# Optimization experiments

Hardware: AMD Instinct MI355X
Metric: run time of the kernel (lower is better)

Reference implementation:

```python
import jax, jax.numpy as jnp
import numpy as np

B, N, D, H, DK, DV = 16, 512, 512, 8, 64, 64


def setup_inputs() -> dict:
    key = jax.random.key(0)
    ks = jax.random.split(key, 16)
    xav = lambda k, fi, fo: jax.random.uniform(k, (fi, fo), jnp.float32,
                                               -jnp.sqrt(6.0 / (fi + fo)), jnp.sqrt(6.0 / (fi + fo)))
    return {
        "queries": jax.random.normal(ks[0], (B, N, D), jnp.float32),
        "keys": jax.random.normal(ks[1], (B, N, D), jnp.float32),
        "values": jax.random.normal(ks[2], (B, N, D), jnp.float32),
        "box_relation_embed_matrix": jax.random.uniform(ks[3], (B, H, N, N), jnp.float32),
        "ExtrAtt": jax.random.normal(ks[4], (B, H, N, N), jnp.float32),
        "Wq": xav(ks[5], D, H * DK), "bq": jnp.zeros((H * DK,), jnp.float32),
        "Wk": xav(ks[6], D, H * DK), "bk": jnp.zeros((H * DK,), jnp.float32),
        "Wv": xav(ks[7], D, H * DV), "bv": jnp.zeros((H * DV,), jnp.float32),
        "Wo": xav(ks[8], H * DV, D), "bo": jnp.zeros((D,), jnp.float32),
    }


def reference(queries, keys, values, box_relation_embed_matrix, ExtrAtt,
              Wq, bq, Wk, bk, Wv, bv, Wo, bo):
    b_s, nq, _ = queries.shape
    nk = keys.shape[1]
    # projections -> [B, H, N, d]
    q = (queries @ Wq + bq).reshape(b_s, nq, H, DK).transpose(0, 2, 1, 3)
    k = (keys @ Wk + bk).reshape(b_s, nk, H, DK).transpose(0, 2, 1, 3)
    v = (values @ Wv + bv).reshape(b_s, nk, H, DV).transpose(0, 2, 1, 3)
    scale = 1.0 / jnp.sqrt(jnp.asarray(DK, queries.dtype))
    att = jnp.einsum('bhqd,bhkd->bhqk', q, k) * scale
    # log geometric (box) bias + content attention, first softmax
    w_mn = jnp.log(jnp.clip(box_relation_embed_matrix, 1e-6, None)) + att
    w_mn = jax.nn.softmax(w_mn, axis=-1)
    # dropout is identity in eval; add extra attention and re-normalize
    att2 = jax.nn.softmax(w_mn + ExtrAtt, axis=-1)
    out = jnp.einsum('bhqk,bhkd->bhqd', att2, v)
    out = out.transpose(0, 2, 1, 3).reshape(b_s, nq, H * DV)
    return out @ Wo + bo
```

## Files before the change

kernel.cpp:

```cpp
#include <hip/hip_runtime.h>
#include <hip/hip_bf16.h>

#define NB 16
#define NN 512
#define ND 512
#define NH 8

using short8 = __attribute__((ext_vector_type(8))) short;
using f32x4  = __attribute__((ext_vector_type(4))) float;

static __device__ __forceinline__ unsigned short f2bf(float f) {
  unsigned u = __builtin_bit_cast(unsigned, f);
  unsigned r = 0x7fffu + ((u >> 16) & 1u);
  return (unsigned short)((u + r) >> 16);
}
static __device__ __forceinline__ float bf2f(unsigned short u) {
  return __builtin_bit_cast(float, (unsigned)u << 16);
}
static __device__ __forceinline__ void ld_lds16(const float* g, float* l) {
  __builtin_amdgcn_global_load_lds((const __attribute__((address_space(1))) void*)g,
                                   (__attribute__((address_space(3))) void*)l, 16, 0, 0);
}

__global__ __launch_bounds__(256) void wprep(
    const float* __restrict__ Wq, const float* __restrict__ Wk,
    const float* __restrict__ Wv, const float* __restrict__ Wo,
    unsigned short* __restrict__ T) {
  const float* W;
  switch (blockIdx.z) {
    case 0: W = Wq; break;
    case 1: W = Wk; break;
    case 2: W = Wv; break;
    default: W = Wo; break;
  }
  unsigned short* Wt = T + (size_t)blockIdx.z * 512 * 512;
  __shared__ float tile[64][65];
  const int t = threadIdx.x;
  const int k0 = blockIdx.x * 64, n0 = blockIdx.y * 64;
#pragma unroll
  for (int it = 0; it < 4; ++it) {
    int row = it * 16 + (t >> 4);
    int c4 = (t & 15) * 4;
    float4 v = *(const float4*)&W[(size_t)(k0 + row) * 512 + n0 + c4];
    tile[row][c4] = v.x; tile[row][c4 + 1] = v.y;
    tile[row][c4 + 2] = v.z; tile[row][c4 + 3] = v.w;
  }
  __syncthreads();
#pragma unroll
  for (int it = 0; it < 4; ++it) {
    int nr = it * 16 + (t >> 4);
    int k4 = (t & 15) * 4;
    ushort4 o;
    o.x = f2bf(tile[k4 + 0][nr]); o.y = f2bf(tile[k4 + 1][nr]);
    o.z = f2bf(tile[k4 + 2][nr]); o.w = f2bf(tile[k4 + 3][nr]);
    *(ushort4*)&Wt[(size_t)(n0 + nr) * 512 + k0 + k4] = o;
  }
}

__global__ __launch_bounds__(256) void qkv_gemm(
    const float* __restrict__ Xq, const float* __restrict__ Xk,
    const float* __restrict__ Xv, const unsigned short* __restrict__ Wt,
    const float* __restrict__ bq, const float* __restrict__ bk,
    const float* __restrict__ bv, unsigned short* __restrict__ q_ws,
    unsigned short* __restrict__ k_ws, unsigned short* __restrict__ vt_ws) {
  const int zi = blockIdx.z;
  const float* X = (zi == 0) ? Xq : (zi == 1) ? Xk : Xv;
  const unsigned short* Wz = Wt + (size_t)zi * 512 * 512;
  const float* bias = (zi == 0) ? bq : (zi == 1) ? bk : bv;
  const int m0 = blockIdx.x * 128, n0 = blockIdx.y * 128;
  __shared__ unsigned short Al[2][128][40];
  __shared__ unsigned short Bl[2][128][40];
  const int t = threadIdx.x;
  const int w = t >> 6, l = t & 63;
  const int lr = l & 15, lg = l >> 4;
  const int wr = (w >> 1) * 64, wc = (w & 1) * 64;
  f32x4 acc[4][4] = {};
  for (int kk = 0; kk < 512; kk += 64) {
    __syncthreads();
    {
      const int colk = (t & 15) * 4;
      const int kc = colk >> 5, kin = colk & 31;
#pragma unroll
      for (int p = 0; p < 8; ++p) {
        int row = p * 16 + (t >> 4);
        float4 v = *(const float4*)&X[(size_t)(m0 + row) * 512 + kk + colk];
        ushort4 o;
        o.x = f2bf(v.x); o.y = f2bf(v.y); o.z = f2bf(v.z); o.w = f2bf(v.w);
        *(ushort4*)&Al[kc][row][kin] = o;
      }
      const int colk8 = (t & 7) * 8;
      const int kc2 = colk8 >> 5, kin2 = colk8 & 31;
#pragma unroll
      for (int p = 0; p < 4; ++p) {
        int row = p * 32 + (t >> 3);
        short8 v = *(const short8*)&Wz[(size_t)(n0 + row) * 512 + kk + colk8];
        *(short8*)&Bl[kc2][row][kin2] = v;
      }
    }
    __syncthreads();
#pragma unroll
    for (int kc = 0; kc < 2; ++kc) {
      short8 a[4], b[4];
      const int lk = lg * 8;
#pragma unroll
      for (int i = 0; i < 4; ++i) a[i] = *(const short8*)&Al[kc][wr + i * 16 + lr][lk];
#pragma unroll
      for (int i = 0; i < 4; ++i) b[i] = *(const short8*)&Bl[kc][wc + i * 16 + lr][lk];
#pragma unroll
      for (int i = 0; i < 4; ++i)
#pragma unroll
        for (int j = 0; j < 4; ++j)
          acc[i][j] = __builtin_amdgcn_mfma_f32_16x16x32_bf16(a[i], b[j], acc[i][j], 0, 0, 0);
    }
  }
#pragma unroll
  for (int j = 0; j < 4; ++j) {
    const int col = n0 + wc + j * 16 + lr;
    const float bb = bias[col];
    const int hh = col >> 6, dv = col & 63;
#pragma unroll
    for (int i = 0; i < 4; ++i) {
      const int mbase = m0 + wr + i * 16 + lg * 4;
      const int b_ = mbase >> 9, nt = mbase & 511;
      if (zi == 2) {
        ushort4 o;
        o.x = f2bf(acc[i][j][0] + bb); o.y = f2bf(acc[i][j][1] + bb);
        o.z = f2bf(acc[i][j][2] + bb); o.w = f2bf(acc[i][j][3] + bb);
        *(ushort4*)&vt_ws[((size_t)(b_ * NH + hh) * 64 + dv) * 512 + nt] = o;
      } else {
        unsigned short* dst = (zi == 0) ? q_ws : k_ws;
#pragma unroll
        for (int r = 0; r < 4; ++r)
          dst[((size_t)(b_ * NH + hh) * 512 + nt + r) * 64 + dv] = f2bf(acc[i][j][r] + bb);
      }
    }
  }
}

__global__ __launch_bounds__(256, 2) void attn_kernel(
    const unsigned short* __restrict__ q_ws, const unsigned short* __restrict__ k_ws,
    const unsigned short* __restrict__ vt_ws, const float* __restrict__ box,
    const float* __restrict__ Ext, unsigned short* __restrict__ hidden) {
  const int t = threadIdx.x;
  const int w = t >> 6, l = t & 63;
  const int lr = l & 15, lg = l >> 4;
  const int wg = blockIdx.x;
  const int xcd = wg & 7, slot = wg >> 3;
  const int bh = xcd + 8 * (slot >> 5);
  const int q0 = (slot & 31) * 16;
  const int b = bh >> 3, h = bh & 7;

  const unsigned short* Qp = q_ws + (size_t)bh * 512 * 64;
  const unsigned short* Kp = k_ws + (size_t)bh * 512 * 64;
  const unsigned short* Vt = vt_ws + (size_t)bh * 64 * 512;
  const float* boxp = box + ((size_t)bh * 512 + q0) * 512;
  const float* Ep = Ext + ((size_t)bh * 512 + q0) * 512;

  __shared__ __align__(16) unsigned char stg[4][16384];
  __shared__ float red[4][16];
  __shared__ float red2[4][16];

  const int n0w = w * 128;
  float* wst = (float*)stg[w];
  float* wstE = (float*)(stg[w] + 8192);
  unsigned short* Pus = (unsigned short*)stg[w];

  short8 qf0 = *(const short8*)&Qp[(size_t)(q0 + lr) * 64 + lg * 8];
  short8 qf1 = *(const short8*)&Qp[(size_t)(q0 + lr) * 64 + 32 + lg * 8];
  short8 kf[8][2];
#pragma unroll
  for (int c = 0; c < 8; ++c) {
    const int krow = n0w + c * 16 + lr;
    kf[c][0] = *(const short8*)&Kp[(size_t)krow * 64 + lg * 8];
    kf[c][1] = *(const short8*)&Kp[(size_t)krow * 64 + 32 + lg * 8];
  }
  __builtin_amdgcn_sched_barrier(0);
#pragma unroll
  for (int c = 0; c < 8; ++c)
    ld_lds16(&boxp[(size_t)(l >> 2) * 512 + n0w + c * 16 + (l & 3) * 4], &wst[c * 256]);
#pragma unroll
  for (int c = 0; c < 8; ++c)
    ld_lds16(&Ep[(size_t)(l >> 2) * 512 + n0w + c * 16 + (l & 3) * 4], &wstE[c * 256]);
  __builtin_amdgcn_sched_barrier(0);

  f32x4 z[8];
#pragma unroll
  for (int c = 0; c < 8; ++c) {
    f32x4 a = {0.f, 0.f, 0.f, 0.f};
    a = __builtin_amdgcn_mfma_f32_16x16x32_bf16(kf[c][0], qf0, a, 0, 0, 0);
    a = __builtin_amdgcn_mfma_f32_16x16x32_bf16(kf[c][1], qf1, a, 0, 0, 0);
    z[c] = a;
  }
  asm volatile("s_waitcnt vmcnt(8)" ::: "memory");
  __builtin_amdgcn_sched_barrier(0);

  float s1 = 0.f;
#pragma unroll
  for (int c = 0; c < 8; ++c) {
    f32x4 bx4 = *(const f32x4*)&wst[c * 256 + lr * 16 + lg * 4];
    float e0 = fmaxf(bx4[0], 1e-6f) * __expf(z[c][0] * 0.125f);
    float e1 = fmaxf(bx4[1], 1e-6f) * __expf(z[c][1] * 0.125f);
    float e2 = fmaxf(bx4[2], 1e-6f) * __expf(z[c][2] * 0.125f);
    float e3 = fmaxf(bx4[3], 1e-6f) * __expf(z[c][3] * 0.125f);
    s1 += (e0 + e1) + (e2 + e3);
    ushort4 o;
    o.x = f2bf(e0); o.y = f2bf(e1); o.z = f2bf(e2); o.w = f2bf(e3);
    *(ushort4*)&Pus[c * 256 + lr * 16 + lg * 4] = o;
  }
  s1 += __shfl_xor(s1, 16);
  s1 += __shfl_xor(s1, 32);
  if (lg == 0) red[w][lr] = s1;
  asm volatile("s_waitcnt lgkmcnt(0)" ::: "memory");
  __builtin_amdgcn_s_barrier();
  const float l1i = 1.0f / (red[0][lr] + red[1][lr] + red[2][lr] + red[3][lr]);
  asm volatile("s_waitcnt vmcnt(0)" ::: "memory");
  __builtin_amdgcn_sched_barrier(0);

  float s2 = 0.f;
#pragma unroll
  for (int c = 0; c < 8; ++c) {
    f32x4 ex4 = *(const f32x4*)&wstE[c * 256 + lr * 16 + lg * 4];
    ushort4 u = *(const ushort4*)&Pus[c * 256 + lr * 16 + lg * 4];
    float e0 = __expf(bf2f(u.x) * l1i + ex4[0]);
    float e1 = __expf(bf2f(u.y) * l1i + ex4[1]);
    float e2 = __expf(bf2f(u.z) * l1i + ex4[2]);
    float e3 = __expf(bf2f(u.w) * l1i + ex4[3]);
    s2 += (e0 + e1) + (e2 + e3);
    ushort4 o;
    o.x = f2bf(e0); o.y = f2bf(e1); o.z = f2bf(e2); o.w = f2bf(e3);
    *(ushort4*)&Pus[c * 256 + lr * 16 + lg * 4] = o;
  }
  s2 += __shfl_xor(s2, 16);
  s2 += __shfl_xor(s2, 32);
  if (lg == 0) red2[w][lr] = s2;
  asm volatile("s_waitcnt lgkmcnt(0)" ::: "memory");
  __builtin_amdgcn_s_barrier();

  f32x4 o4[4] = {};
#pragma unroll
  for (int kc = 0; kc < 4; ++kc) {
    short8 pa = *(const short8*)&Pus[(kc * 2 + (lg >> 1)) * 256 + lr * 16 + (lg & 1) * 8];
#pragma unroll
    for (int c2 = 0; c2 < 4; ++c2) {
      short8 vf = *(const short8*)&Vt[(size_t)(c2 * 16 + lr) * 512 + n0w + kc * 32 + lg * 8];
      o4[c2] = __builtin_amdgcn_mfma_f32_16x16x32_bf16(pa, vf, o4[c2], 0, 0, 0);
    }
  }
  f32x4 rs = *(const f32x4*)&red2[0][lg * 4];
#pragma unroll
  for (int w2 = 1; w2 < 4; ++w2) {
    f32x4 p = *(const f32x4*)&red2[w2][lg * 4];
#pragma unroll
    for (int r = 0; r < 4; ++r) rs[r] += p[r];
  }
  f32x4 l2v;
#pragma unroll
  for (int r = 0; r < 4; ++r) l2v[r] = 1.0f / rs[r];
  float* ow = (float*)stg[w];
#pragma unroll
  for (int c2 = 0; c2 < 4; ++c2)
#pragma unroll
    for (int r = 0; r < 4; ++r)
      ow[(lg * 4 + r) * 68 + c2 * 16 + lr] = o4[c2][r] * l2v[r];
  asm volatile("s_waitcnt lgkmcnt(0)" ::: "memory");
  __builtin_amdgcn_s_barrier();
  {
    const int lrow = t >> 4;
    const int d4 = (t & 15) * 4;
    f32x4 s = *(const f32x4*)&((const float*)stg[0])[lrow * 68 + d4];
#pragma unroll
    for (int w2 = 1; w2 < 4; ++w2) {
      f32x4 p = *(const f32x4*)&((const float*)stg[w2])[lrow * 68 + d4];
#pragma unroll
      for (int r = 0; r < 4; ++r) s[r] += p[r];
    }
    ushort4 oo;
    oo.x = f2bf(s[0]); oo.y = f2bf(s[1]); oo.z = f2bf(s[2]); oo.w = f2bf(s[3]);
    *(ushort4*)&hidden[(size_t)(b * 512 + q0 + lrow) * 512 + h * 64 + d4] = oo;
  }
}

__global__ __launch_bounds__(256) void out_gemm(
    const unsigned short* __restrict__ hidden, const unsigned short* __restrict__ WoT,
    const float* __restrict__ bo, float* __restrict__ out) {
  const int m0 = blockIdx.x * 128, n0 = blockIdx.y * 128;
  __shared__ unsigned short Al[2][128][40];
  __shared__ unsigned short Bl[2][128][40];
  const int t = threadIdx.x;
  const int w = t >> 6, l = t & 63;
  const int lr = l & 15, lg = l >> 4;
  const int wr = (w >> 1) * 64, wc = (w & 1) * 64;
  f32x4 acc[4][4] = {};
  for (int kk = 0; kk < 512; kk += 64) {
    __syncthreads();
    {
      const int colk8 = (t & 7) * 8;
      const int kc2 = colk8 >> 5, kin2 = colk8 & 31;
#pragma unroll
      for (int p = 0; p < 4; ++p) {
        int row = p * 32 + (t >> 3);
        short8 v = *(const short8*)&hidden[(size_t)(m0 + row) * 512 + kk + colk8];
        *(short8*)&Al[kc2][row][kin2] = v;
      }
#pragma unroll
      for (int p = 0; p < 4; ++p) {
        int row = p * 32 + (t >> 3);
        short8 v = *(const short8*)&WoT[(size_t)(n0 + row) * 512 + kk + colk8];
        *(short8*)&Bl[kc2][row][kin2] = v;
      }
    }
    __syncthreads();
#pragma unroll
    for (int kc = 0; kc < 2; ++kc) {
      short8 a[4], b[4];
      const int lk = lg * 8;
#pragma unroll
      for (int i = 0; i < 4; ++i) a[i] = *(const short8*)&Al[kc][wr + i * 16 + lr][lk];
#pragma unroll
      for (int i = 0; i < 4; ++i) b[i] = *(const short8*)&Bl[kc][wc + i * 16 + lr][lk];
#pragma unroll
      for (int i = 0; i < 4; ++i)
#pragma unroll
        for (int j = 0; j < 4; ++j)
          acc[i][j] = __builtin_amdgcn_mfma_f32_16x16x32_bf16(a[i], b[j], acc[i][j], 0, 0, 0);
    }
  }
#pragma unroll
  for (int j = 0; j < 4; ++j) {
    const int col = n0 + wc + j * 16 + lr;
    const float bb = bo[col];
#pragma unroll
    for (int i = 0; i < 4; ++i)
#pragma unroll
      for (int r = 0; r < 4; ++r)
        out[(size_t)(m0 + wr + i * 16 + lg * 4 + r) * 512 + col] = acc[i][j][r] + bb;
  }
}

extern "C" void kernel_launch(void* const* d_in, const int* in_sizes, int n_in,
                              void* d_out, int out_size, void* d_ws, size_t ws_size,
                              hipStream_t stream) {
  const float* queries = (const float*)d_in[0];
  const float* keys = (const float*)d_in[1];
  const float* values = (const float*)d_in[2];
  const float* box = (const float*)d_in[3];
  const float* ext = (const float*)d_in[4];
  const float* Wq = (const float*)d_in[5];
  const float* bq = (const float*)d_in[6];
  const float* Wk = (const float*)d_in[7];
  const float* bk = (const float*)d_in[8];
  const float* Wv = (const float*)d_in[9];
  const float* bv = (const float*)d_in[10];
  const float* Wo = (const float*)d_in[11];
  const float* bo = (const float*)d_in[12];
  float* out = (float*)d_out;

  char* ws = (char*)d_ws;
  unsigned short* q_ws = (unsigned short*)(ws);
  unsigned short* k_ws = (unsigned short*)(ws + 8u * 1024 * 1024);
  unsigned short* vt_ws = (unsigned short*)(ws + 16u * 1024 * 1024);
  unsigned short* hidden = (unsigned short*)(ws + 24u * 1024 * 1024);
  unsigned short* wt = (unsigned short*)(ws + 32u * 1024 * 1024);

  wprep<<<dim3(8, 8, 4), 256, 0, stream>>>(Wq, Wk, Wv, Wo, wt);
  qkv_gemm<<<dim3(64, 4, 3), 256, 0, stream>>>(queries, keys, values, wt, bq, bk, bv,
                                               q_ws, k_ws, vt_ws);
  attn_kernel<<<dim3(4096), 256, 0, stream>>>(q_ws, k_ws, vt_ws, box, ext, hidden);
  out_gemm<<<dim3(64, 4), 256, 0, stream>>>(hidden, wt + 3u * 512 * 512, bo, out);
}
```

Baseline: 164.6 us.

## Load box/ExtrAtt into registers instead of LDS staging, cut LDS for occupancy

Replaces the async global-to-LDS staging of the box and extra-attention tiles with direct dwordx4 register loads in MFMA output layout. Softmax intermediates stay in fp32 registers rather than round-tripping through bf16 in LDS, and the second normalization is applied to P before the PV MFMA. LDS per block shrinks from 64KB to about 18KB and launch bounds rise to 3 blocks per SIMD for higher occupancy. The trade-offs are register pressure from the 16 f32x4 arrays, and losing the overlap of the ExtrAtt load with the first phase that LDS staging gave.

```diff
diff --git a/kernel.cpp b/kernel.cpp
--- a/kernel.cpp
+++ b/kernel.cpp
@@ -14,13 +14,10 @@
   unsigned r = 0x7fffu + ((u >> 16) & 1u);
   return (unsigned short)((u + r) >> 16);
 }
-static __device__ __forceinline__ float bf2f(unsigned short u) {
-  return __builtin_bit_cast(float, (unsigned)u << 16);
-}
-static __device__ __forceinline__ void ld_lds16(const float* g, float* l) {
-  __builtin_amdgcn_global_load_lds((const __attribute__((address_space(1))) void*)g,
-                                   (__attribute__((address_space(3))) void*)l, 16, 0, 0);
-}
+
+#define LDX(dst, base, offlit)                                          \
+  asm volatile("global_load_dwordx4 %0, %1, off" offlit                 \
+               : "=v"(dst) : "v"(base) : "memory")
 
 __global__ __launch_bounds__(256) void wprep(
     const float* __restrict__ Wq, const float* __restrict__ Wk,
@@ -137,7 +134,7 @@
   }
 }
 
-__global__ __launch_bounds__(256, 2) void attn_kernel(
+__global__ __launch_bounds__(256, 3) void attn_kernel(
     const unsigned short* __restrict__ q_ws, const unsigned short* __restrict__ k_ws,
     const unsigned short* __restrict__ vt_ws, const float* __restrict__ box,
     const float* __restrict__ Ext, unsigned short* __restrict__ hidden) {
@@ -156,15 +153,25 @@
   const float* boxp = box + ((size_t)bh * 512 + q0) * 512;
   const float* Ep = Ext + ((size_t)bh * 512 + q0) * 512;
 
-  __shared__ __align__(16) unsigned char stg[4][16384];
   __shared__ float red[4][16];
   __shared__ float red2[4][16];
+  __shared__ __align__(16) unsigned char wsh[4][4608];
 
   const int n0w = w * 128;
-  float* wst = (float*)stg[w];
-  float* wstE = (float*)(stg[w] + 8192);
-  unsigned short* Pus = (unsigned short*)stg[w];
-
+  unsigned short(*Pw)[144] = (unsigned short(*)[144])wsh[w];
+
+  f32x4 bx[8];
+  {
+    const float* bp = boxp + (size_t)lr * 512 + n0w + lg * 4;
+    LDX(bx[0], bp, "");
+    LDX(bx[1], bp, " offset:64");
+    LDX(bx[2], bp, " offset:128");
+    LDX(bx[3], bp, " offset:192");
+    LDX(bx[4], bp, " offset:256");
+    LDX(bx[5], bp, " offset:320");
+    LDX(bx[6], bp, " offset:384");
+    LDX(bx[7], bp, " offset:448");
+  }
   short8 qf0 = *(const short8*)&Qp[(size_t)(q0 + lr) * 64 + lg * 8];
   short8 qf1 = *(const short8*)&Qp[(size_t)(q0 + lr) * 64 + 32 + lg * 8];
   short8 kf[8][2];
@@ -174,42 +181,39 @@
     kf[c][0] = *(const short8*)&Kp[(size_t)krow * 64 + lg * 8];
     kf[c][1] = *(const short8*)&Kp[(size_t)krow * 64 + 32 + lg * 8];
   }
+  asm volatile("s_waitcnt vmcnt(0)" ::: "memory");
   __builtin_amdgcn_sched_barrier(0);
-#pragma unroll
-  for (int c = 0; c < 8; ++c)
-    ld_lds16(&boxp[(size_t)(l >> 2) * 512 + n0w + c * 16 + (l & 3) * 4], &wst[c * 256]);
-#pragma unroll
-  for (int c = 0; c < 8; ++c)
-    ld_lds16(&Ep[(size_t)(l >> 2) * 512 + n0w + c * 16 + (l & 3) * 4], &wstE[c * 256]);
-  __builtin_amdgcn_sched_barrier(0);
 
   f32x4 z[8];
+  float s1 = 0.f;
 #pragma unroll
   for (int c = 0; c < 8; ++c) {
     f32x4 a = {0.f, 0.f, 0.f, 0.f};
     a = __builtin_amdgcn_mfma_f32_16x16x32_bf16(kf[c][0], qf0, a, 0, 0, 0);
     a = __builtin_amdgcn_mfma_f32_16x16x32_bf16(kf[c][1], qf1, a, 0, 0, 0);
-    z[c] = a;
-  }
-  asm volatile("s_waitcnt vmcnt(8)" ::: "memory");
-  __builtin_amdgcn_sched_barrier(0);
-
-  float s1 = 0.f;
-#pragma unroll
-  for (int c = 0; c < 8; ++c) {
-    f32x4 bx4 = *(const f32x4*)&wst[c * 256 + lr * 16 + lg * 4];
-    float e0 = fmaxf(bx4[0], 1e-6f) * __expf(z[c][0] * 0.125f);
-    float e1 = fmaxf(bx4[1], 1e-6f) * __expf(z[c][1] * 0.125f);
-    float e2 = fmaxf(bx4[2], 1e-6f) * __expf(z[c][2] * 0.125f);
-    float e3 = fmaxf(bx4[3], 1e-6f) * __expf(z[c][3] * 0.125f);
-    s1 += (e0 + e1) + (e2 + e3);
-    ushort4 o;
-    o.x = f2bf(e0); o.y = f2bf(e1); o.z = f2bf(e2); o.w = f2bf(e3);
-    *(ushort4*)&Pus[c * 256 + lr * 16 + lg * 4] = o;
+    f32x4 e;
+    e[0] = fmaxf(bx[c][0], 1e-6f) * __expf(a[0] * 0.125f);
+    e[1] = fmaxf(bx[c][1], 1e-6f) * __expf(a[1] * 0.125f);
+    e[2] = fmaxf(bx[c][2], 1e-6f) * __expf(a[2] * 0.125f);
+    e[3] = fmaxf(bx[c][3], 1e-6f) * __expf(a[3] * 0.125f);
+    s1 += (e[0] + e[1]) + (e[2] + e[3]);
+    z[c] = e;
   }
   s1 += __shfl_xor(s1, 16);
   s1 += __shfl_xor(s1, 32);
   if (lg == 0) red[w][lr] = s1;
+  f32x4 ex[8];
+  {
+    const float* ep = Ep + (size_t)lr * 512 + n0w + lg * 4;
+    LDX(ex[0], ep, "");
+    LDX(ex[1], ep, " offset:64");
+    LDX(ex[2], ep, " offset:128");
+    LDX(ex[3], ep, " offset:192");
+    LDX(ex[4], ep, " offset:256");
+    LDX(ex[5], ep, " offset:320");
+    LDX(ex[6], ep, " offset:384");
+    LDX(ex[7], ep, " offset:448");
+  }
   asm volatile("s_waitcnt lgkmcnt(0)" ::: "memory");
   __builtin_amdgcn_s_barrier();
   const float l1i = 1.0f / (red[0][lr] + red[1][lr] + red[2][lr] + red[3][lr]);
@@ -219,58 +223,55 @@
   float s2 = 0.f;
 #pragma unroll
   for (int c = 0; c < 8; ++c) {
-    f32x4 ex4 = *(const f32x4*)&wstE[c * 256 + lr * 16 + lg * 4];
-    ushort4 u = *(const ushort4*)&Pus[c * 256 + lr * 16 + lg * 4];
-    float e0 = __expf(bf2f(u.x) * l1i + ex4[0]);
-    float e1 = __expf(bf2f(u.y) * l1i + ex4[1]);
-    float e2 = __expf(bf2f(u.z) * l1i + ex4[2]);
-    float e3 = __expf(bf2f(u.w) * l1i + ex4[3]);
-    s2 += (e0 + e1) + (e2 + e3);
-    ushort4 o;
-    o.x = f2bf(e0); o.y = f2bf(e1); o.z = f2bf(e2); o.w = f2bf(e3);
-    *(ushort4*)&Pus[c * 256 + lr * 16 + lg * 4] = o;
+    f32x4 e;
+    e[0] = __expf(z[c][0] * l1i + ex[c][0]);
+    e[1] = __expf(z[c][1] * l1i + ex[c][1]);
+    e[2] = __expf(z[c][2] * l1i + ex[c][2]);
+    e[3] = __expf(z[c][3] * l1i + ex[c][3]);
+    s2 += (e[0] + e[1]) + (e[2] + e[3]);
+    z[c] = e;
   }
   s2 += __shfl_xor(s2, 16);
   s2 += __shfl_xor(s2, 32);
   if (lg == 0) red2[w][lr] = s2;
   asm volatile("s_waitcnt lgkmcnt(0)" ::: "memory");
   __builtin_amdgcn_s_barrier();
-
+  const float l2i = 1.0f / (red2[0][lr] + red2[1][lr] + red2[2][lr] + red2[3][lr]);
+
+#pragma unroll
+  for (int c = 0; c < 8; ++c) {
+    ushort4 o;
+    o.x = f2bf(z[c][0] * l2i);
+    o.y = f2bf(z[c][1] * l2i);
+    o.z = f2bf(z[c][2] * l2i);
+    o.w = f2bf(z[c][3] * l2i);
+    *(ushort4*)&Pw[lr][c * 16 + lg * 4] = o;
+  }
   f32x4 o4[4] = {};
 #pragma unroll
   for (int kc = 0; kc < 4; ++kc) {
-    short8 pa = *(const short8*)&Pus[(kc * 2 + (lg >> 1)) * 256 + lr * 16 + (lg & 1) * 8];
+    short8 pa = *(const short8*)&Pw[lr][kc * 32 + lg * 8];
 #pragma unroll
     for (int c2 = 0; c2 < 4; ++c2) {
       short8 vf = *(const short8*)&Vt[(size_t)(c2 * 16 + lr) * 512 + n0w + kc * 32 + lg * 8];
       o4[c2] = __builtin_amdgcn_mfma_f32_16x16x32_bf16(pa, vf, o4[c2], 0, 0, 0);
     }
   }
-  f32x4 rs = *(const f32x4*)&red2[0][lg * 4];
-#pragma unroll
-  for (int w2 = 1; w2 < 4; ++w2) {
-    f32x4 p = *(const f32x4*)&red2[w2][lg * 4];
-#pragma unroll
-    for (int r = 0; r < 4; ++r) rs[r] += p[r];
-  }
-  f32x4 l2v;
-#pragma unroll
-  for (int r = 0; r < 4; ++r) l2v[r] = 1.0f / rs[r];
-  float* ow = (float*)stg[w];
+  float* ow = (float*)wsh[w];
 #pragma unroll
   for (int c2 = 0; c2 < 4; ++c2)
 #pragma unroll
     for (int r = 0; r < 4; ++r)
-      ow[(lg * 4 + r) * 68 + c2 * 16 + lr] = o4[c2][r] * l2v[r];
+      ow[(lg * 4 + r) * 68 + c2 * 16 + lr] = o4[c2][r];
   asm volatile("s_waitcnt lgkmcnt(0)" ::: "memory");
   __builtin_amdgcn_s_barrier();
   {
     const int lrow = t >> 4;
     const int d4 = (t & 15) * 4;
-    f32x4 s = *(const f32x4*)&((const float*)stg[0])[lrow * 68 + d4];
+    f32x4 s = *(const f32x4*)&((const float*)wsh[0])[lrow * 68 + d4];
 #pragma unroll
     for (int w2 = 1; w2 < 4; ++w2) {
-      f32x4 p = *(const f32x4*)&((const float*)stg[w2])[lrow * 68 + d4];
+      f32x4 p = *(const f32x4*)&((const float*)wsh[w2])[lrow * 68 + d4];
 #pragma unroll
       for (int r = 0; r < 4; ++r) s[r] += p[r];
     }
```

Result: no change. 165.8 us (+0.7%).
